# Optimization experiments

Measured on AMD Instinct MI355X. Metric: run time of the kernel, lower is better.

Reference implementation:

```python
import jax, jax.numpy as jnp
import numpy as np

DIM = 1024
DEPTH = 6
HEADS = 16
DH = 64
INNER = HEADS * DH  # 1024
MLP = 4096
B, N = 2, 2048
SCALE = DH ** (-0.5)  # 0.125; module divides softmax output by this (x8)
EPS = 1e-5


def setup_inputs() -> dict:
    key = jax.random.key(0)
    ks = jax.random.split(key, 5)
    s = jnp.float32(0.02)
    return {
        "x": jax.random.normal(ks[0], (B, N, DIM), dtype=jnp.float32),
        "ln1_g": jnp.ones((DEPTH, DIM), jnp.float32),
        "ln1_b": jnp.zeros((DEPTH, DIM), jnp.float32),
        "w_qkv": jax.random.normal(ks[1], (DEPTH, DIM, 3 * INNER), jnp.float32) * s,
        "w_out": jax.random.normal(ks[2], (DEPTH, INNER, DIM), jnp.float32) * s,
        "b_out": jnp.zeros((DEPTH, DIM), jnp.float32),
        "ln2_g": jnp.ones((DEPTH, DIM), jnp.float32),
        "ln2_b": jnp.zeros((DEPTH, DIM), jnp.float32),
        "w1": jax.random.normal(ks[3], (DEPTH, DIM, MLP), jnp.float32) * s,
        "b1": jnp.zeros((DEPTH, MLP), jnp.float32),
        "w2": jax.random.normal(ks[4], (DEPTH, MLP, DIM), jnp.float32) * s,
        "b2": jnp.zeros((DEPTH, DIM), jnp.float32),
    }


def _layernorm(x, g, b):
    m = x.mean(-1, keepdims=True)
    v = ((x - m) ** 2).mean(-1, keepdims=True)
    return (x - m) * jax.lax.rsqrt(v + EPS) * g + b


def _attention(x, w_qkv, w_out, b_out):
    b, n, _ = x.shape
    qkv = x @ w_qkv  # [b, n, 3*inner]
    q, k, v = jnp.split(qkv, 3, axis=-1)

    def heads(t):
        return t.reshape(b, n, HEADS, DH).transpose(0, 2, 1, 3)  # [b,h,n,d]

    q, k, v = heads(q), heads(k), heads(v)
    # Faithful to source: softmax of UNSCALED logits, then divide by scale.
    score = jax.nn.softmax(jnp.einsum("bhqd,bhkd->bhqk", q, k), axis=-1) / SCALE
    o = jnp.einsum("bhqk,bhkd->bhqd", score, v)
    o = o.transpose(0, 2, 1, 3).reshape(b, n, INNER)
    return o @ w_out + b_out


def reference(x, ln1_g, ln1_b, w_qkv, w_out, b_out, ln2_g, ln2_b, w1, b1, w2, b2):
    def layer(h, p):
        g1, bb1, wq, wo, bo, g2, bb2, ww1, bw1, ww2, bw2 = p
        h = h + _attention(_layernorm(h, g1, bb1), wq, wo, bo)
        f = _layernorm(h, g2, bb2) @ ww1 + bw1
        f = jax.nn.gelu(f, approximate=False)  # nn.GELU default = exact erf
        h = h + f @ ww2 + bw2
        return h, None

    out, _ = jax.lax.scan(
        layer, x, (ln1_g, ln1_b, w_qkv, w_out, b_out, ln2_g, ln2_b, w1, b1, w2, b2)
    )
    return out
```

## Files before the change

### kernel.cpp

```cpp
#include <hip/hip_runtime.h>
#include <cstdint>

typedef __attribute__((ext_vector_type(4))) float f32x4;
typedef __attribute__((ext_vector_type(8))) short short8;
typedef __attribute__((ext_vector_type(4))) short short4v;
typedef _Float16 half8v __attribute__((ext_vector_type(8)));

__device__ __forceinline__ unsigned short f2h(float x) {
  _Float16 h = (_Float16)x;
  return __builtin_bit_cast(unsigned short, h);
}
__device__ __forceinline__ unsigned int pk2(float a, float b) {
  auto h = __builtin_amdgcn_cvt_pkrtz(a, b);
  return __builtin_bit_cast(unsigned int, h);
}

template <typename V>
__device__ __forceinline__ auto mfma_impl(V a, V b, f32x4 c, int)
    -> decltype(__builtin_amdgcn_mfma_f32_16x16x32_f16(a, b, c, 0, 0, 0)) {
  return __builtin_amdgcn_mfma_f32_16x16x32_f16(a, b, c, 0, 0, 0);
}
template <typename V>
__device__ __forceinline__ f32x4 mfma_impl(V a, V b, f32x4 c, long) {
  return __builtin_amdgcn_mfma_f32_16x16x32_f16(
      __builtin_bit_cast(half8v, a), __builtin_bit_cast(half8v, b), c, 0, 0, 0);
}
__device__ __forceinline__ f32x4 MFMA(short8 a, short8 b, f32x4 c) {
  return mfma_impl(a, b, c, 0);
}

__device__ __forceinline__ void load_lds16(const void* g, void* l) {
  __builtin_amdgcn_global_load_lds(
      (__attribute__((address_space(1))) void*)(uintptr_t)g,
      (__attribute__((address_space(3))) void*)l, 16, 0, 0);
}

__global__ __launch_bounds__(256) void ln_f16_kernel(
    const float* __restrict__ X, const float* __restrict__ gam,
    const float* __restrict__ bet, unsigned short* __restrict__ Y) {
  __shared__ float red[8];
  const int row = blockIdx.x, t = threadIdx.x;
  const float4 v = ((const float4*)(X + (size_t)row * 1024))[t];
  float s = v.x + v.y + v.z + v.w;
#pragma unroll
  for (int o = 32; o >= 1; o >>= 1) s += __shfl_xor(s, o, 64);
  if ((t & 63) == 0) red[t >> 6] = s;
  __syncthreads();
  const float mean = (red[0] + red[1] + red[2] + red[3]) * (1.0f / 1024.0f);
  const float dx = v.x - mean, dy = v.y - mean, dz = v.z - mean, dw = v.w - mean;
  float ss = dx * dx + dy * dy + dz * dz + dw * dw;
#pragma unroll
  for (int o = 32; o >= 1; o >>= 1) ss += __shfl_xor(ss, o, 64);
  if ((t & 63) == 0) red[4 + (t >> 6)] = ss;
  __syncthreads();
  const float var = (red[4] + red[5] + red[6] + red[7]) * (1.0f / 1024.0f);
  const float rstd = rsqrtf(var + 1e-5f);
  const float4 gg = ((const float4*)gam)[t];
  const float4 bb = ((const float4*)bet)[t];
  ushort4 o4;
  o4.x = f2h(dx * rstd * gg.x + bb.x);
  o4.y = f2h(dy * rstd * gg.y + bb.y);
  o4.z = f2h(dz * rstd * gg.z + bb.z);
  o4.w = f2h(dw * rstd * gg.w + bb.w);
  ((ushort4*)(Y + (size_t)row * 1024))[t] = o4;
}

__global__ __launch_bounds__(256) void transpose_all_kernel(
    const float* __restrict__ wq, const float* __restrict__ wo,
    const float* __restrict__ w1, const float* __restrict__ w2,
    unsigned short* __restrict__ wtq, unsigned short* __restrict__ wto,
    unsigned short* __restrict__ wt1, unsigned short* __restrict__ wt2) {
  __shared__ float t[32][33];
  int i = blockIdx.x;
  const float* W; unsigned short* WT; int K, N;
  if (i < 3072)      { W = wq; WT = wtq; K = 1024; N = 3072; }
  else if (i < 4096) { i -= 3072; W = wo; WT = wto; K = 1024; N = 1024; }
  else if (i < 8192) { i -= 4096; W = w1; WT = wt1; K = 1024; N = 4096; }
  else               { i -= 8192; W = w2; WT = wt2; K = 4096; N = 1024; }
  const int nt = N >> 5;
  const int n0 = (i % nt) * 32, k0 = (i / nt) * 32;
  const int tx = threadIdx.x, ty = threadIdx.y;
#pragma unroll
  for (int j = 0; j < 4; ++j)
    t[ty + 8 * j][tx] = W[(size_t)(k0 + ty + 8 * j) * N + n0 + tx];
  __syncthreads();
#pragma unroll
  for (int j = 0; j < 4; ++j)
    WT[(size_t)(n0 + ty + 8 * j) * K + k0 + tx] = f2h(t[tx][ty + 8 * j]);
}

__global__ __launch_bounds__(256) void vt_transpose_kernel(
    const unsigned short* __restrict__ qkvb, unsigned short* __restrict__ VT) {
  __shared__ unsigned short t[32][33];
  const int c0 = blockIdx.x * 32;
  const int r0 = blockIdx.y * 32;
  const int b = blockIdx.z;
  const int tx = threadIdx.x, ty = threadIdx.y;
  const size_t base = (size_t)b * 2048;
#pragma unroll
  for (int i = 0; i < 4; ++i)
    t[ty + 8 * i][tx] = qkvb[(base + r0 + ty + 8 * i) * 3072 + 2048 + c0 + tx];
  __syncthreads();
#pragma unroll
  for (int i = 0; i < 4; ++i)
    VT[((size_t)b * 1024 + c0 + ty + 8 * i) * 2048 + r0 + tx] = t[tx][ty + 8 * i];
}

template <int BM, int EPI>
__global__ __launch_bounds__(256, BM == 64 ? 3 : 2) void gemm_f16_kernel(
    const unsigned short* __restrict__ A, const unsigned short* __restrict__ BT,
    void* Cout, const float* __restrict__ bias, const float* __restrict__ res,
    int M, int N, int K) {
  constexpr int BN = 128, BK = 64;
  constexpr int MR = BM / 32;
  constexpr int ACH = BM * BK / 8;
  constexpr int BCH = BN * BK / 8;
  __shared__ alignas(16) unsigned short a_sh[2][BM * BK];
  __shared__ alignas(16) unsigned short b_sh[2][BN * BK];
  const int tid = threadIdx.x;
  const int w = tid >> 6, lane = tid & 63, g = lane >> 4, lm = lane & 15;
  const int m0 = blockIdx.y * BM, n0 = blockIdx.x * BN;
  const int wm = (w >> 1) * (BM / 2), wn = (w & 1) * 64;
  f32x4 acc[MR][4] = {};
  const int nsteps = K >> 6;

  auto stage = [&](int buf, int kk) {
#pragma unroll
    for (int c0 = 0; c0 < ACH; c0 += 256) {
      const int c = c0 + tid, row = c >> 3;
      const int sc = (c & 7) ^ (row & 7);
      const int cb = c0 + (tid & 192);
      load_lds16(A + (size_t)(m0 + row) * K + kk + sc * 8, &a_sh[buf][cb * 8]);
    }
#pragma unroll
    for (int c0 = 0; c0 < BCH; c0 += 256) {
      const int c = c0 + tid, row = c >> 3;
      const int sc = (c & 7) ^ (row & 7);
      const int cb = c0 + (tid & 192);
      load_lds16(BT + (size_t)(n0 + row) * K + kk + sc * 8, &b_sh[buf][cb * 8]);
    }
  };

  stage(0, 0);
  __syncthreads();
  int cur = 0;
  for (int step = 0; step < nsteps; ++step) {
    if (step + 1 < nsteps) stage(cur ^ 1, (step + 1) * BK);
#pragma unroll
    for (int kc = 0; kc < 2; ++kc) {
      short8 af[MR], bfr[4];
#pragma unroll
      for (int i = 0; i < MR; ++i) {
        const int r = wm + i * 16 + lm;
        af[i] = *(const short8*)&a_sh[cur][r * 64 + (((kc << 2) | g) ^ (r & 7)) * 8];
      }
#pragma unroll
      for (int j = 0; j < 4; ++j) {
        const int r = wn + j * 16 + lm;
        bfr[j] = *(const short8*)&b_sh[cur][r * 64 + (((kc << 2) | g) ^ (r & 7)) * 8];
      }
#pragma unroll
      for (int i = 0; i < MR; ++i)
#pragma unroll
        for (int j = 0; j < 4; ++j)
          acc[i][j] = MFMA(af[i], bfr[j], acc[i][j]);
    }
    if (step + 1 < nsteps) {
      __syncthreads();
      cur ^= 1;
    }
  }

#pragma unroll
  for (int i = 0; i < MR; ++i) {
    const int row = m0 + wm + i * 16 + g * 4;
#pragma unroll
    for (int j = 0; j < 4; ++j) {
      const int col = n0 + wn + j * 16 + lm;
#pragma unroll
      for (int r = 0; r < 4; ++r) {
        const float v = acc[i][j][r];
        const size_t idx = (size_t)(row + r) * N + col;
        if (EPI == 0) {
          ((unsigned short*)Cout)[idx] = f2h(v);
        } else if (EPI == 1) {
          const float xx = v + bias[col];
          ((unsigned short*)Cout)[idx] =
              f2h(0.5f * xx * (1.0f + erff(xx * 0.70710678118654752f)));
        } else {
          ((float*)Cout)[idx] = res[idx] + v + bias[col];
        }
      }
    }
  }
}

__global__ __launch_bounds__(512) void attn_kernel(
    const unsigned short* __restrict__ qkv, const unsigned short* __restrict__ vt,
    unsigned short* __restrict__ obuf) {
  constexpr int PK = 72;
  constexpr int PV = 68;
  __shared__ alignas(16) unsigned short Ks[64 * PK];
  __shared__ alignas(16) unsigned short VsT[64 * PV];
  const int tid = threadIdx.x;
  const int w = tid >> 6, lane = tid & 63, g = lane >> 4, lm = lane & 15;
  const int qbase = blockIdx.x * 128, h = blockIdx.y, b = blockIdx.z;
  const size_t rowbase = (size_t)b * 2048;
  const int r0 = tid >> 3, cc = tid & 7;

  const unsigned short* qp =
      qkv + (rowbase + qbase + w * 16 + lm) * 3072 + h * 64 + g * 8;
  short8 qf[2];
  qf[0] = *(const short8*)qp;
  qf[1] = *(const short8*)(qp + 32);

  const unsigned short* kptr = qkv + (rowbase + r0) * 3072 + 1024 + h * 64 + cc * 8;
  const unsigned short* vtp = vt + ((size_t)b * 1024 + h * 64 + r0) * 2048 + cc * 8;
  uint4 kreg, vreg;
  auto load_tile = [&](int n) {
    kreg = *(const uint4*)(kptr + (size_t)n * 64 * 3072);
    vreg = *(const uint4*)(vtp + n * 64);
  };
  auto write_tile = [&]() {
    *(uint4*)&Ks[r0 * PK + cc * 8] = kreg;
    *(uint4*)&VsT[r0 * PV + cc * 8] = vreg;
  };

  load_tile(0);
  float mrun = -1e30f, lrun = 0.0f;
  f32x4 accO[4] = {};

  for (int n = 0; n < 32; ++n) {
    __syncthreads();
    write_tile();
    __syncthreads();
    if (n + 1 < 32) load_tile(n + 1);

    f32x4 sf[4] = {};
    __builtin_amdgcn_s_setprio(1);
#pragma unroll
    for (int s2 = 0; s2 < 2; ++s2)
#pragma unroll
      for (int i = 0; i < 4; ++i) {
        const short8 kf = *(const short8*)&Ks[(i * 16 + lm) * PK + s2 * 32 + g * 8];
        sf[i] = MFMA(kf, qf[s2], sf[i]);
      }
    __builtin_amdgcn_s_setprio(0);

    float tmax = -1e30f;
#pragma unroll
    for (int i = 0; i < 4; ++i)
#pragma unroll
      for (int r = 0; r < 4; ++r) tmax = fmaxf(tmax, sf[i][r]);
    tmax = fmaxf(tmax, __shfl_xor(tmax, 16, 64));
    tmax = fmaxf(tmax, __shfl_xor(tmax, 32, 64));
    const float mnew = fmaxf(mrun, tmax);
    const float scale = __expf(mrun - mnew);
    float p[4][4];
    float psum = 0.0f;
#pragma unroll
    for (int i = 0; i < 4; ++i)
#pragma unroll
      for (int r = 0; r < 4; ++r) {
        p[i][r] = __expf(sf[i][r] - mnew);
        psum += p[i][r];
      }
    psum += __shfl_xor(psum, 16, 64);
    psum += __shfl_xor(psum, 32, 64);
    lrun = lrun * scale + psum;
    mrun = mnew;
#pragma unroll
    for (int t = 0; t < 4; ++t) accO[t] = accO[t] * scale;

    uint4 pbu[2];
#pragma unroll
    for (int blk = 0; blk < 2; ++blk) {
      pbu[blk].x = pk2(p[2 * blk][0], p[2 * blk][1]);
      pbu[blk].y = pk2(p[2 * blk][2], p[2 * blk][3]);
      pbu[blk].z = pk2(p[2 * blk + 1][0], p[2 * blk + 1][1]);
      pbu[blk].w = pk2(p[2 * blk + 1][2], p[2 * blk + 1][3]);
    }

    __builtin_amdgcn_s_setprio(1);
#pragma unroll
    for (int blk = 0; blk < 2; ++blk) {
      const short8 pbv = __builtin_bit_cast(short8, pbu[blk]);
#pragma unroll
      for (int t = 0; t < 4; ++t) {
        const int base = (16 * t + lm) * PV + 32 * blk + 4 * g;
        const short4v vlo = *(const short4v*)&VsT[base];
        const short4v vhi = *(const short4v*)&VsT[base + 16];
        const short8 vf = {vlo[0], vlo[1], vlo[2], vlo[3],
                           vhi[0], vhi[1], vhi[2], vhi[3]};
        accO[t] = MFMA(vf, pbv, accO[t]);
      }
    }
    __builtin_amdgcn_s_setprio(0);
  }

  const float inv = 8.0f / lrun;
  const size_t orow = rowbase + qbase + w * 16 + lm;
#pragma unroll
  for (int t = 0; t < 4; ++t) {
    ushort4 o4;
    o4.x = f2h(accO[t][0] * inv);
    o4.y = f2h(accO[t][1] * inv);
    o4.z = f2h(accO[t][2] * inv);
    o4.w = f2h(accO[t][3] * inv);
    *(ushort4*)&obuf[orow * 1024 + h * 64 + t * 16 + g * 4] = o4;
  }
}

extern "C" void kernel_launch(void* const* d_in, const int* in_sizes, int n_in,
                              void* d_out, int out_size, void* d_ws, size_t ws_size,
                              hipStream_t stream) {
  const float* x     = (const float*)d_in[0];
  const float* ln1_g = (const float*)d_in[1];
  const float* ln1_b = (const float*)d_in[2];
  const float* w_qkv = (const float*)d_in[3];
  const float* w_out = (const float*)d_in[4];
  const float* b_out = (const float*)d_in[5];
  const float* ln2_g = (const float*)d_in[6];
  const float* ln2_b = (const float*)d_in[7];
  const float* w1    = (const float*)d_in[8];
  const float* b1    = (const float*)d_in[9];
  const float* w2    = (const float*)d_in[10];
  const float* b2    = (const float*)d_in[11];
  float* h = (float*)d_out;

  char* ws = (char*)d_ws;
  const size_t MB = 1u << 20;
  unsigned short* xn   = (unsigned short*)(ws);
  unsigned short* ob   = (unsigned short*)(ws + 8 * MB);
  unsigned short* qkvb = (unsigned short*)(ws + 16 * MB);
  unsigned short* mid  = (unsigned short*)(ws + 40 * MB);
  unsigned short* wt   = (unsigned short*)(ws + 72 * MB);
  unsigned short* wtq = wt;
  unsigned short* wto = wt + 3145728;
  unsigned short* wt1 = wt + 4194304;
  unsigned short* wt2 = wt + 8388608;

  hipError_t e0 = hipMemcpyAsync(h, x, (size_t)4096 * 1024 * sizeof(float),
                                 hipMemcpyDeviceToDevice, stream);
  (void)e0;

  const dim3 tb(32, 8);
  for (int L = 0; L < 6; ++L) {
    const float* Lg1 = ln1_g + L * 1024;
    const float* Lb1 = ln1_b + L * 1024;
    const float* Lwq = w_qkv + (size_t)L * 1024 * 3072;
    const float* Lwo = w_out + (size_t)L * 1024 * 1024;
    const float* Lbo = b_out + L * 1024;
    const float* Lg2 = ln2_g + L * 1024;
    const float* Lb2 = ln2_b + L * 1024;
    const float* Lw1 = w1 + (size_t)L * 1024 * 4096;
    const float* Lb1m = b1 + L * 4096;
    const float* Lw2 = w2 + (size_t)L * 4096 * 1024;
    const float* Lb2m = b2 + L * 1024;

    transpose_all_kernel<<<12288, tb, 0, stream>>>(
        Lwq, Lwo, Lw1, Lw2, wtq, wto, wt1, wt2);

    ln_f16_kernel<<<4096, 256, 0, stream>>>(h, Lg1, Lb1, xn);
    gemm_f16_kernel<128, 0><<<dim3(24, 32), 256, 0, stream>>>(
        xn, wtq, qkvb, nullptr, nullptr, 4096, 3072, 1024);
    vt_transpose_kernel<<<dim3(32, 64, 2), tb, 0, stream>>>(qkvb, xn);
    attn_kernel<<<dim3(16, 16, 2), 512, 0, stream>>>(qkvb, xn, ob);
    gemm_f16_kernel<64, 2><<<dim3(8, 64), 256, 0, stream>>>(
        ob, wto, h, Lbo, h, 4096, 1024, 1024);

    ln_f16_kernel<<<4096, 256, 0, stream>>>(h, Lg2, Lb2, xn);
    gemm_f16_kernel<128, 1><<<dim3(32, 32), 256, 0, stream>>>(
        xn, wt1, mid, Lb1m, nullptr, 4096, 4096, 1024);
    gemm_f16_kernel<64, 2><<<dim3(8, 64), 256, 0, stream>>>(
        mid, wt2, h, Lb2m, h, 4096, 1024, 4096);
  }
  (void)in_sizes; (void)n_in; (void)out_size; (void)ws_size;
}
```

Baseline: 1.620 ms.

## Fuse V transpose into QKV GEMM epilogue, remap GEMM blocks, enlarge attention blocks

The QKV GEMM now writes the V columns directly in transposed layout into a scratch buffer, which removes the separate V-transpose kernel and its extra global memory round trip. All GEMMs switch to a 1D grid with a block-index swizzle that spreads consecutive block IDs across 8 groups, likely aimed at the XCD layout and cache locality. The attention kernel doubles to 1024 threads and 256 queries per block, with half the threads loading K and half loading V, which halves K/V reloads per query. The risks are lower occupancy in attention and strided 8-byte stores in the transposed V write.

```diff
diff --git a/kernel.cpp b/kernel.cpp
--- a/kernel.cpp
+++ b/kernel.cpp
@@ -89,28 +89,11 @@
     WT[(size_t)(n0 + ty + 8 * j) * K + k0 + tx] = f2h(t[tx][ty + 8 * j]);
 }
 
-__global__ __launch_bounds__(256) void vt_transpose_kernel(
-    const unsigned short* __restrict__ qkvb, unsigned short* __restrict__ VT) {
-  __shared__ unsigned short t[32][33];
-  const int c0 = blockIdx.x * 32;
-  const int r0 = blockIdx.y * 32;
-  const int b = blockIdx.z;
-  const int tx = threadIdx.x, ty = threadIdx.y;
-  const size_t base = (size_t)b * 2048;
-#pragma unroll
-  for (int i = 0; i < 4; ++i)
-    t[ty + 8 * i][tx] = qkvb[(base + r0 + ty + 8 * i) * 3072 + 2048 + c0 + tx];
-  __syncthreads();
-#pragma unroll
-  for (int i = 0; i < 4; ++i)
-    VT[((size_t)b * 1024 + c0 + ty + 8 * i) * 2048 + r0 + tx] = t[tx][ty + 8 * i];
-}
-
 template <int BM, int EPI>
 __global__ __launch_bounds__(256, BM == 64 ? 3 : 2) void gemm_f16_kernel(
     const unsigned short* __restrict__ A, const unsigned short* __restrict__ BT,
     void* Cout, const float* __restrict__ bias, const float* __restrict__ res,
-    int M, int N, int K) {
+    unsigned short* __restrict__ vtout, int gx, int M, int N, int K) {
   constexpr int BN = 128, BK = 64;
   constexpr int MR = BM / 32;
   constexpr int ACH = BM * BK / 8;
@@ -119,7 +102,10 @@
   __shared__ alignas(16) unsigned short b_sh[2][BN * BK];
   const int tid = threadIdx.x;
   const int w = tid >> 6, lane = tid & 63, g = lane >> 4, lm = lane & 15;
-  const int m0 = blockIdx.y * BM, n0 = blockIdx.x * BN;
+  int bid = blockIdx.x;
+  const int cpx = gridDim.x >> 3;
+  bid = (bid & 7) * cpx + (bid >> 3);
+  const int m0 = (bid / gx) * BM, n0 = (bid % gx) * BN;
   const int wm = (w >> 1) * (BM / 2), wn = (w & 1) * 64;
   f32x4 acc[MR][4] = {};
   const int nsteps = K >> 6;
@@ -171,6 +157,25 @@
     }
   }
 
+  if (EPI == 3 && n0 >= 2048) {
+#pragma unroll
+    for (int i = 0; i < MR; ++i) {
+      const int row = m0 + wm + i * 16 + g * 4;
+      const int bb = row >> 11, rin = row & 2047;
+#pragma unroll
+      for (int j = 0; j < 4; ++j) {
+        const int vcol = n0 + wn + j * 16 + lm - 2048;
+        ushort4 o4;
+        o4.x = f2h(acc[i][j][0]);
+        o4.y = f2h(acc[i][j][1]);
+        o4.z = f2h(acc[i][j][2]);
+        o4.w = f2h(acc[i][j][3]);
+        *(ushort4*)&vtout[((size_t)bb * 1024 + vcol) * 2048 + rin] = o4;
+      }
+    }
+    return;
+  }
+
 #pragma unroll
   for (int i = 0; i < MR; ++i) {
     const int row = m0 + wm + i * 16 + g * 4;
@@ -181,7 +186,7 @@
       for (int r = 0; r < 4; ++r) {
         const float v = acc[i][j][r];
         const size_t idx = (size_t)(row + r) * N + col;
-        if (EPI == 0) {
+        if (EPI == 0 || EPI == 3) {
           ((unsigned short*)Cout)[idx] = f2h(v);
         } else if (EPI == 1) {
           const float xx = v + bias[col];
@@ -195,7 +200,7 @@
   }
 }
 
-__global__ __launch_bounds__(512) void attn_kernel(
+__global__ __launch_bounds__(1024) void attn_kernel(
     const unsigned short* __restrict__ qkv, const unsigned short* __restrict__ vt,
     unsigned short* __restrict__ obuf) {
   constexpr int PK = 72;
@@ -204,9 +209,10 @@
   __shared__ alignas(16) unsigned short VsT[64 * PV];
   const int tid = threadIdx.x;
   const int w = tid >> 6, lane = tid & 63, g = lane >> 4, lm = lane & 15;
-  const int qbase = blockIdx.x * 128, h = blockIdx.y, b = blockIdx.z;
+  const int qbase = blockIdx.x * 256, h = blockIdx.y, b = blockIdx.z;
   const size_t rowbase = (size_t)b * 2048;
-  const int r0 = tid >> 3, cc = tid & 7;
+  const int sr = (tid & 511) >> 3, sc = tid & 7;
+  const bool doK = tid < 512;
 
   const unsigned short* qp =
       qkv + (rowbase + qbase + w * 16 + lm) * 3072 + h * 64 + g * 8;
@@ -214,17 +220,17 @@
   qf[0] = *(const short8*)qp;
   qf[1] = *(const short8*)(qp + 32);
 
-  const unsigned short* kptr = qkv + (rowbase + r0) * 3072 + 1024 + h * 64 + cc * 8;
-  const unsigned short* vtp = vt + ((size_t)b * 1024 + h * 64 + r0) * 2048 + cc * 8;
-  uint4 kreg, vreg;
+  const unsigned short* sptr = doK
+      ? qkv + (rowbase + sr) * 3072 + 1024 + h * 64 + sc * 8
+      : vt + ((size_t)b * 1024 + h * 64 + sr) * 2048 + sc * 8;
+  const int sdst = doK ? sr * PK + sc * 8 : sr * PV + sc * 8;
+  unsigned short* sbase = doK ? Ks : VsT;
+  uint4 sreg;
   auto load_tile = [&](int n) {
-    kreg = *(const uint4*)(kptr + (size_t)n * 64 * 3072);
-    vreg = *(const uint4*)(vtp + n * 64);
+    sreg = doK ? *(const uint4*)(sptr + (size_t)n * 64 * 3072)
+               : *(const uint4*)(sptr + n * 64);
   };
-  auto write_tile = [&]() {
-    *(uint4*)&Ks[r0 * PK + cc * 8] = kreg;
-    *(uint4*)&VsT[r0 * PV + cc * 8] = vreg;
-  };
+  auto write_tile = [&]() { *(uint4*)&sbase[sdst] = sreg; };
 
   load_tile(0);
   float mrun = -1e30f, lrun = 0.0f;
@@ -362,18 +368,17 @@
         Lwq, Lwo, Lw1, Lw2, wtq, wto, wt1, wt2);
 
     ln_f16_kernel<<<4096, 256, 0, stream>>>(h, Lg1, Lb1, xn);
-    gemm_f16_kernel<128, 0><<<dim3(24, 32), 256, 0, stream>>>(
-        xn, wtq, qkvb, nullptr, nullptr, 4096, 3072, 1024);
-    vt_transpose_kernel<<<dim3(32, 64, 2), tb, 0, stream>>>(qkvb, xn);
-    attn_kernel<<<dim3(16, 16, 2), 512, 0, stream>>>(qkvb, xn, ob);
-    gemm_f16_kernel<64, 2><<<dim3(8, 64), 256, 0, stream>>>(
-        ob, wto, h, Lbo, h, 4096, 1024, 1024);
+    gemm_f16_kernel<128, 3><<<768, 256, 0, stream>>>(
+        xn, wtq, qkvb, nullptr, nullptr, mid, 24, 4096, 3072, 1024);
+    attn_kernel<<<dim3(8, 16, 2), 1024, 0, stream>>>(qkvb, mid, ob);
+    gemm_f16_kernel<64, 2><<<512, 256, 0, stream>>>(
+        ob, wto, h, Lbo, h, nullptr, 8, 4096, 1024, 1024);
 
     ln_f16_kernel<<<4096, 256, 0, stream>>>(h, Lg2, Lb2, xn);
-    gemm_f16_kernel<128, 1><<<dim3(32, 32), 256, 0, stream>>>(
-        xn, wt1, mid, Lb1m, nullptr, 4096, 4096, 1024);
-    gemm_f16_kernel<64, 2><<<dim3(8, 64), 256, 0, stream>>>(
-        mid, wt2, h, Lb2m, h, 4096, 1024, 4096);
+    gemm_f16_kernel<128, 1><<<1024, 256, 0, stream>>>(
+        xn, wt1, mid, Lb1m, nullptr, nullptr, 32, 4096, 4096, 1024);
+    gemm_f16_kernel<64, 2><<<512, 256, 0, stream>>>(
+        mid, wt2, h, Lb2m, h, nullptr, 8, 4096, 1024, 4096);
   }
   (void)in_sizes; (void)n_in; (void)out_size; (void)ws_size;
 }
```

Measured after the change: 1.614 ms. Within noise of the previous version (-0.3%).
